# Kernel tuning notes

Measured on AMD Instinct MI355X. Metric: run time of the kernel, lower is better.

Reference implementation:

```python
import jax, jax.numpy as jnp
import numpy as np

DIM = 1536   # model dim
H = 12       # heads
HD = 128     # head dim
S = 3072     # tokens
BLK = 128    # tokens per attention block (window partition size)
NB = S // BLK  # 24 blocks
BH, BW = 6, 4  # spatial block grid (BH*BW == NB, one frame)
WIN = 6      # local window in blocks
TOPK = 128   # top-k block pairs kept per (head, frame)
EPS = 1e-5
SCALE = 1.0 / np.sqrt(HD)


def rmsnorm(x, g):
    return x * jax.lax.rsqrt(jnp.mean(x * x, axis=-1, keepdims=True) + EPS) * g


def rope(x, cos, sin):
    # x: [B,S,DIM]; cos/sin: [S,1,HD//2] -> complex rotation on (real,imag) pairs
    b, s, _ = x.shape
    x = x.reshape(b, s, H, HD // 2, 2)
    xr, xi = x[..., 0], x[..., 1]
    c, sn = cos[None], sin[None]            # [1,S,1,HD//2]
    yr = xr * c - xi * sn
    yi = xr * sn + xi * c
    return jnp.stack([yr, yi], axis=-1).reshape(b, s, H * HD)


def local_block_mask(bh, bw, win):
    # build_local_block_mask_shifted_vec_normal_slide (static, numpy)
    r, c = np.arange(bh), np.arange(bw)
    YY, XX = np.meshgrid(r, c, indexing='ij')
    ra, ca = YY.reshape(-1), XX.reshape(-1)
    hh, hw = win // 2, win // 2
    sr, sc = ra - hh, ca - hw
    er, ec = sr + win - 1, sc + win - 1
    in_r = (ra[None, :] >= sr[:, None]) & (ra[None, :] <= er[:, None])
    in_c = (ca[None, :] >= sc[:, None]) & (ca[None, :] <= ec[:, None])
    return jnp.asarray(in_r & in_c)  # [NB,NB] bool


LOCAL = local_block_mask(BH, BW, WIN)


def draft_block_mask(q, k):
    # generate_draft_block_mask: pooled-QK softmax + per-(head,frame) top-k threshold
    qw = q[0].reshape(NB, BLK, DIM).mean(axis=1)   # [NB,DIM] avgpool over window
    kw = k[0].reshape(NB, BLK, DIM).mean(axis=1)
    qh = qw.reshape(NB, H, HD).transpose(1, 0, 2)  # [H,NB,HD]
    kh = kw.reshape(NB, H, HD).transpose(1, 0, 2)
    scores = jnp.einsum('hld,hmd->hlm', qh, kh) * SCALE  # [H,NB,NB]
    rl, rn = NB // LOCAL.shape[0], NB // LOCAL.shape[1]
    lm = jnp.tile(LOCAL, (rl, rn))                       # [NB,NB]
    scores = jnp.where(lm[None], scores, -jnp.inf)
    attn = jax.nn.softmax(scores, axis=-1)               # rows include self -> finite
    it = 1  # one frame: NB == BH*BW
    flat = attn.reshape(H * it, -1)                      # [H, NB*NB]
    k_top = min(flat.shape[1] - 1, TOPK)
    thr = jax.lax.top_k(flat, k_top + 1)[0][:, -1:]      # (topk+1)-th value
    return (flat > thr).reshape(H, NB, NB)               # bool block mask


def forward(x, wq, bq, wk, bk, wv, bv, wo, bo, gq, gk, freqs_cos, freqs_sin):
    q = rope(rmsnorm(x @ wq.T + bq, gq), freqs_cos, freqs_sin)
    k = rope(rmsnorm(x @ wk.T + bk, gk), freqs_cos, freqs_sin)
    v = x @ wv.T + bv

    bm = jax.lax.stop_gradient(draft_block_mask(q, k))   # [H,NB,NB] (no-grad in torch)
    tok = jnp.repeat(jnp.repeat(bm, BLK, axis=1), BLK, axis=2)  # [H,S,S] token mask

    qh = q.reshape(1, S, H, HD).transpose(0, 2, 1, 3)
    kh = k.reshape(1, S, H, HD).transpose(0, 2, 1, 3)
    vh = v.reshape(1, S, H, HD).transpose(0, 2, 1, 3)

    s = jnp.einsum('bhsd,bhtd->bhst', qh, kh) * SCALE
    s = jnp.where(tok[None], s, -jnp.inf)
    m = jnp.max(s, axis=-1, keepdims=True)
    m = jnp.where(jnp.isfinite(m), m, 0.0)               # guard fully-masked rows
    p = jnp.exp(s - m) * tok[None].astype(s.dtype)
    den = jnp.sum(p, axis=-1, keepdims=True)
    o = jnp.einsum('bhst,bhtd->bhsd', p, vh) / jnp.where(den > 0, den, 1.0)
    o = o.transpose(0, 2, 1, 3).reshape(1, S, DIM)
    return o @ wo.T + bo


def setup_inputs() -> dict:
    key = jax.random.key(0)
    ks = jax.random.split(key, 8)
    w = lambda kk: (jax.random.normal(kk, (DIM, DIM), jnp.float32) * 0.02)
    pos = jnp.arange(S, dtype=jnp.float32)
    inv = 1.0 / (10000.0 ** (jnp.arange(HD // 2, dtype=jnp.float32) / (HD // 2)))
    ang = pos[:, None] * inv[None, :]                    # [S,HD//2]
    return {
        'x': jax.random.normal(ks[0], (1, S, DIM), jnp.float32),
        'wq': w(ks[1]), 'bq': jnp.zeros((DIM,), jnp.float32),
        'wk': w(ks[2]), 'bk': jnp.zeros((DIM,), jnp.float32),
        'wv': w(ks[3]), 'bv': jnp.zeros((DIM,), jnp.float32),
        'wo': w(ks[4]), 'bo': jnp.zeros((DIM,), jnp.float32),
        'gq': jnp.ones((DIM,), jnp.float32),
        'gk': jnp.ones((DIM,), jnp.float32),
        'freqs_cos': jnp.cos(ang)[:, None, :],
        'freqs_sin': jnp.sin(ang)[:, None, :],
    }


def reference(x, wq, bq, wk, bk, wv, bv, wo, bo, gq, gk, freqs_cos, freqs_sin):
    return forward(x, wq, bq, wk, bk, wv, bv, wo, bo, gq, gk, freqs_cos, freqs_sin)
```

## Files before the change

### kernel.cpp

```cpp
#include <hip/hip_runtime.h>
#include <hip/hip_bf16.h>
#include <math.h>

#define SEQ 3072
#define DIM 1536
#define NH 12
#define HD 128
#define NB 24
#define BLKT 128
#define NBSQ 576
#define TOPK_N 128
#define EPSV 1e-5f
#define SCALEV 0.08838834764831845f

typedef __attribute__((ext_vector_type(8))) short short8;
typedef __attribute__((ext_vector_type(4))) short short4v;
typedef __attribute__((ext_vector_type(4))) float f32x4;

typedef __attribute__((address_space(1))) void* gas1_t;
typedef __attribute__((address_space(3))) void* las3_t;

__device__ __forceinline__ float b2f(short u) {
  return __uint_as_float(((unsigned int)(unsigned short)u) << 16);
}
__device__ __forceinline__ short f2b(float x) {
  __hip_bfloat16 h = __float2bfloat16(x);
  return *reinterpret_cast<short*>(&h);
}
__device__ __forceinline__ float ldin(const void* p, size_t i, int f32) {
  return f32 ? ((const float*)p)[i] : b2f(((const short*)p)[i]);
}
__device__ __forceinline__ void gload_lds16(const void* g, void* l) {
  __builtin_amdgcn_global_load_lds((gas1_t)g, (las3_t)l, 16, 0, 0);
}

__global__ __launch_bounds__(256)
void dtype_probe(const void* __restrict__ w, int* __restrict__ flag) {
  __shared__ int cnt;
  if (threadIdx.x == 0) cnt = 0;
  __syncthreads();
  const short* p = (const short*)w;
  int local = 0;
  for (int i = threadIdx.x; i < 4096; i += 256) {
    float v = b2f(p[i]);
    if (!(fabsf(v) <= 1e3f)) local++;
  }
  atomicAdd(&cnt, local);
  __syncthreads();
  if (threadIdx.x == 0) { flag[0] = (cnt > 16) ? 1 : 0; flag[1] = 0; }
}

__device__ __forceinline__ short8 ldchunk(const void* __restrict__ p, size_t idx, int f32) {
  if (f32) {
    const float* q = (const float*)p + idx;
    f32x4 a = *(const f32x4*)q;
    f32x4 b = *(const f32x4*)(q + 4);
    short8 r;
    r[0] = f2b(a[0]); r[1] = f2b(a[1]); r[2] = f2b(a[2]); r[3] = f2b(a[3]);
    r[4] = f2b(b[0]); r[5] = f2b(b[1]); r[6] = f2b(b[2]); r[7] = f2b(b[3]);
    return r;
  }
  return *(const short8*)((const short*)p + idx);
}

__global__ __launch_bounds__(256)
void cvt_bf16(const void* __restrict__ in, short* __restrict__ out, int n8,
              const int* __restrict__ f) {
  int i = blockIdx.x * 256 + threadIdx.x;
  if (i >= n8) return;
  *(short8*)(out + (size_t)i * 8) = ldchunk(in, (size_t)i * 8, *f);
}

#define BK 64

__global__ __launch_bounds__(256)
void gemm128(const short* __restrict__ A,
             const void* __restrict__ W0, const void* __restrict__ W1, const void* __restrict__ W2,
             const void* __restrict__ b0, const void* __restrict__ b1, const void* __restrict__ b2,
             void* __restrict__ C0, void* __restrict__ C1, void* __restrict__ C2,
             int useWB, const int* __restrict__ wfp, const int* __restrict__ ofp) {
  const int fW = *wfp, fO = *ofp;
  __shared__ __attribute__((aligned(16))) short As[128 * BK];
  __shared__ __attribute__((aligned(16))) short Bs[128 * BK];
  const int tid = threadIdx.x;
  const int w = tid >> 6, lane = tid & 63;
  const int lo = lane & 15, hi = lane >> 4;
  const int wr = w >> 1, wc = w & 1;
  const int bx = blockIdx.x;
  const int wsel = bx / 12;
  const int col0 = (bx - wsel * 12) * 128;
  const int row0 = blockIdx.y * 128;
  const void* W = (wsel == 0) ? W0 : ((wsel == 1) ? W1 : W2);
  const void* bb = (wsel == 0) ? b0 : ((wsel == 1) ? b1 : b2);
  void* C = (wsel == 0) ? C0 : ((wsel == 1) ? C1 : C2);

  const f32x4 zero = {0.f, 0.f, 0.f, 0.f};
  f32x4 acc[4][4];
#pragma unroll
  for (int i = 0; i < 4; i++)
#pragma unroll
    for (int j = 0; j < 4; j++) acc[i][j] = zero;

  for (int k0 = 0; k0 < DIM; k0 += BK) {
#pragma unroll
    for (int i = 0; i < 4; i++) {
      int id = i * 256 + tid;
      int r = id >> 3, c = id & 7;
      gload_lds16(A + (size_t)(row0 + r) * DIM + k0 + (c ^ (r & 7)) * 8, &As[id * 8]);
    }
    if (useWB) {
#pragma unroll
      for (int i = 0; i < 4; i++) {
        int id = i * 256 + tid;
        int r = id >> 3, c = id & 7;
        gload_lds16((const short*)W + (size_t)(col0 + r) * DIM + k0 + (c ^ (r & 7)) * 8,
                    &Bs[id * 8]);
      }
    } else {
#pragma unroll
      for (int i = 0; i < 4; i++) {
        int id = i * 256 + tid;
        int r = id >> 3, c = id & 7;
        short8 v = ldchunk(W, (size_t)(col0 + r) * DIM + k0 + c * 8, fW);
        *(short8*)&Bs[r * BK + 8 * (c ^ (r & 7))] = v;
      }
    }
    __syncthreads();
#pragma unroll
    for (int kk = 0; kk < 2; kk++) {
      short8 av[4], bv[4];
#pragma unroll
      for (int mi = 0; mi < 4; mi++) {
        int r = wr * 64 + mi * 16 + lo;
        av[mi] = *(const short8*)&As[r * BK + 8 * ((kk * 4 + hi) ^ (r & 7))];
      }
#pragma unroll
      for (int ni = 0; ni < 4; ni++) {
        int r = wc * 64 + ni * 16 + lo;
        bv[ni] = *(const short8*)&Bs[r * BK + 8 * ((kk * 4 + hi) ^ (r & 7))];
      }
#pragma unroll
      for (int mi = 0; mi < 4; mi++)
#pragma unroll
        for (int ni = 0; ni < 4; ni++)
          acc[mi][ni] = __builtin_amdgcn_mfma_f32_16x16x32_bf16(av[mi], bv[ni], acc[mi][ni], 0, 0, 0);
    }
    __syncthreads();
  }

#pragma unroll
  for (int ni = 0; ni < 4; ni++) {
    int col = col0 + wc * 64 + ni * 16 + lo;
    float bias = ldin(bb, col, fW);
#pragma unroll
    for (int mi = 0; mi < 4; mi++) {
      int rowb = row0 + wr * 64 + mi * 16 + hi * 4;
#pragma unroll
      for (int g = 0; g < 4; g++) {
        float v = acc[mi][ni][g] + bias;
        size_t oi = (size_t)(rowb + g) * DIM + col;
        if (fO) ((float*)C)[oi] = v;
        else    ((short*)C)[oi] = f2b(v);
      }
    }
  }
}

__global__ __launch_bounds__(256)
void rmsnorm_rope_kernel(short* __restrict__ x, const void* __restrict__ g,
                         const void* __restrict__ cs, const void* __restrict__ sn,
                         const int* __restrict__ f) {
  const int fI = *f;
  const int s = blockIdx.x, tid = threadIdx.x;
  short* row = x + (size_t)s * DIM;
  short8 rv = {};
  float ss = 0.f;
  if (tid < 192) {
    rv = *(const short8*)(row + tid * 8);
#pragma unroll
    for (int j = 0; j < 8; j++) { float v = b2f(rv[j]); ss += v * v; }
  }
#pragma unroll
  for (int m = 32; m; m >>= 1) ss += __shfl_xor(ss, m, 64);
  __shared__ float wsum[4];
  if ((tid & 63) == 0) wsum[tid >> 6] = ss;
  __syncthreads();
  float rn = rsqrtf((wsum[0] + wsum[1] + wsum[2] + wsum[3]) * (1.0f / DIM) + EPSV);
  if (tid >= 192) return;
  short8 out;
#pragma unroll
  for (int j = 0; j < 4; j++) {
    int p = tid * 4 + j, pi = p & 63;
    float c  = ldin(cs, (size_t)s * 64 + pi, fI);
    float si = ldin(sn, (size_t)s * 64 + pi, fI);
    float xr = b2f(rv[2 * j])     * rn * ldin(g, tid * 8 + 2 * j, fI);
    float xi = b2f(rv[2 * j + 1]) * rn * ldin(g, tid * 8 + 2 * j + 1, fI);
    out[2 * j]     = f2b(xr * c - xi * si);
    out[2 * j + 1] = f2b(xr * si + xi * c);
  }
  *(short8*)(row + tid * 8) = out;
}

__global__ __launch_bounds__(256)
void pool_kernel(const short* __restrict__ x, float* __restrict__ out) {
  const int nb = blockIdx.x;
  const int d = blockIdx.y * 256 + threadIdx.x;
  float s = 0.f;
  for (int t = 0; t < BLKT; t++) s += b2f(x[(size_t)(nb * BLKT + t) * DIM + d]);
  out[nb * DIM + d] = s * (1.0f / BLKT);
}

__global__ __launch_bounds__(256)
void draft_mask_kernel(const float* __restrict__ qw, const float* __restrict__ kw,
                       int* __restrict__ bm) {
  const int h = blockIdx.x, tid = threadIdx.x;
  __shared__ float qh[NB][HD];
  __shared__ float kh[NB][HD];
  __shared__ float attn[NBSQ];
  __shared__ int cw[4];

  for (int idx = tid; idx < NB * HD; idx += 256) {
    int l = idx >> 7, d = idx & 127;
    qh[l][d] = qw[l * DIM + h * HD + d];
    kh[l][d] = kw[l * DIM + h * HD + d];
  }
  __syncthreads();

  for (int idx = tid; idx < NBSQ; idx += 256) {
    int l = idx / NB, m = idx % NB;
    int rl = l >> 2, cl = l & 3, rm = m >> 2, cm = m & 3;
    bool loc = (rm >= rl - 3) && (rm <= rl + 2) && (cm >= cl - 3) && (cm <= cl + 2);
    float sc;
    if (loc) {
      sc = 0.f;
      for (int d = 0; d < HD; d++) sc += qh[l][d] * kh[m][d];
      sc *= SCALEV;
    } else {
      sc = -INFINITY;
    }
    attn[idx] = sc;
  }
  __syncthreads();

  if (tid < NB) {
    float mx = -INFINITY;
    for (int m = 0; m < NB; m++) mx = fmaxf(mx, attn[tid * NB + m]);
    float sm = 0.f;
    for (int m = 0; m < NB; m++) {
      float p = expf(attn[tid * NB + m] - mx);
      attn[tid * NB + m] = p;
      sm += p;
    }
    float inv = 1.0f / sm;
    for (int m = 0; m < NB; m++) attn[tid * NB + m] *= inv;
  }
  __syncthreads();

  unsigned int blo = 0u, bhi = 0x3F800000u;
  while (blo < bhi) {
    unsigned int mid = (blo + bhi) >> 1;
    float t = __uint_as_float(mid);
    int c = 0;
    for (int idx = tid; idx < NBSQ; idx += 256) c += (attn[idx] > t) ? 1 : 0;
#pragma unroll
    for (int m = 1; m < 64; m <<= 1) c += __shfl_xor(c, m, 64);
    if ((tid & 63) == 0) cw[tid >> 6] = c;
    __syncthreads();
    int tot = cw[0] + cw[1] + cw[2] + cw[3];
    if (tot <= TOPK_N) bhi = mid; else blo = mid + 1;
    __syncthreads();
  }
  float thr = __uint_as_float(blo);

  for (int idx = tid; idx < NBSQ; idx += 256)
    bm[h * NBSQ + idx] = (attn[idx] > thr) ? 1 : 0;
}

__global__ __launch_bounds__(256)
void transpose_kernel(const short* __restrict__ v, short* __restrict__ vt) {
  __shared__ short tile[64][68];
  const int s0 = blockIdx.x * 64, c0 = blockIdx.y * 64;
  const int tid = threadIdx.x;
#pragma unroll
  for (int i = 0; i < 4; i++) {
    int id = i * 256 + tid;
    int r = id >> 4, cq = (id & 15) * 4;
    *(short4v*)&tile[r][cq] = *(const short4v*)(v + (size_t)(s0 + r) * DIM + c0 + cq);
  }
  __syncthreads();
#pragma unroll
  for (int i = 0; i < 4; i++) {
    int id = i * 256 + tid;
    int d = id >> 4, sq = (id & 15) * 4;
    short4v val;
#pragma unroll
    for (int jj = 0; jj < 4; jj++) val[jj] = tile[sq + jj][d];
    *(short4v*)(vt + (size_t)(c0 + d) * SEQ + s0 + sq) = val;
  }
}

__global__ __launch_bounds__(512)
void attn_mfma(const short* __restrict__ q, const short* __restrict__ k,
               const short* __restrict__ vt, const int* __restrict__ bm,
               short* __restrict__ o, int* __restrict__ ctr) {
  const int xcd = blockIdx.x & 7;
  const int tid = threadIdx.x;
  const int w = tid >> 6;
  const int lane = tid & 63;
  const int lo = lane & 15, hi = lane >> 4;

  __shared__ __attribute__((aligned(16))) short Ks[128 * 128];
  __shared__ __attribute__((aligned(16))) short Vs[128 * 128];
  __shared__ __attribute__((aligned(16))) short Ps[8][16 * 128];
  __shared__ int tsh;

  const f32x4 zero = {0.f, 0.f, 0.f, 0.f};
  const int sr = tid >> 4, sc = tid & 15;

  for (;;) {
    if (tid == 0) tsh = atomicAdd(&ctr[xcd * 8], 1);
    __syncthreads();
    const int slot = tsh;
    if (slot >= 36) break;
    const int task = xcd * 36 + slot;
    const int h = task / NB;
    const int qb = task - h * NB;

    const int* bmrow = bm + h * NBSQ + qb * NB;
    const short* kh = k + h * HD;
    const short* vth = vt + (size_t)h * HD * SEQ;

    const int qt = qb * 8 + w;
    const int qrow = qt * 16 + lo;
    short8 qa[4];
#pragma unroll
    for (int kk = 0; kk < 4; kk++)
      qa[kk] = *(const short8*)(q + (size_t)qrow * DIM + h * HD + kk * 32 + hi * 8);

    f32x4 oacc[8];
#pragma unroll
    for (int i = 0; i < 8; i++) oacc[i] = zero;
    float m_i[4] = {-INFINITY, -INFINITY, -INFINITY, -INFINITY};
    float l_i[4] = {0.f, 0.f, 0.f, 0.f};

    short8 kreg[4], vreg[4];
    int jc = 0;
    while (jc < NB && !bmrow[jc]) jc++;
    if (jc < NB) {
      const int t0 = jc * BLKT;
#pragma unroll
      for (int i = 0; i < 4; i++) {
        int r = i * 32 + sr;
        kreg[i] = *(const short8*)(kh + (size_t)(t0 + r) * DIM + sc * 8);
        vreg[i] = *(const short8*)(vth + (size_t)r * SEQ + t0 + sc * 8);
      }
    }

    while (jc < NB) {
#pragma unroll
      for (int i = 0; i < 4; i++) {
        int r = i * 32 + sr;
        *(short8*)&Ks[r * 128 + 8 * (sc ^ (r & 7))] = kreg[i];
        *(short8*)&Vs[r * 128 + 8 * (sc ^ (r & 7))] = vreg[i];
      }
      __syncthreads();

      int jn = jc + 1;
      while (jn < NB && !bmrow[jn]) jn++;
      if (jn < NB) {
        const int t0 = jn * BLKT;
#pragma unroll
        for (int i = 0; i < 4; i++) {
          int r = i * 32 + sr;
          kreg[i] = *(const short8*)(kh + (size_t)(t0 + r) * DIM + sc * 8);
          vreg[i] = *(const short8*)(vth + (size_t)r * SEQ + t0 + sc * 8);
        }
      }

      f32x4 S[8];
#pragma unroll
      for (int tt = 0; tt < 8; tt++) {
        f32x4 s = zero;
#pragma unroll
        for (int kk = 0; kk < 4; kk++) {
          int rt = tt * 16 + lo;
          short8 kb = *(const short8*)&Ks[rt * 128 + 8 * ((kk * 4 + hi) ^ (rt & 7))];
          s = __builtin_amdgcn_mfma_f32_16x16x32_bf16(qa[kk], kb, s, 0, 0, 0);
        }
        S[tt] = s;
      }

      float alpha[4];
#pragma unroll
      for (int g = 0; g < 4; g++) {
        float mx = S[0][g];
#pragma unroll
        for (int tt = 1; tt < 8; tt++) mx = fmaxf(mx, S[tt][g]);
#pragma unroll
        for (int msk = 1; msk < 16; msk <<= 1) mx = fmaxf(mx, __shfl_xor(mx, msk, 16));
        mx *= SCALEV;
        float mn = fmaxf(m_i[g], mx);
        alpha[g] = __expf(m_i[g] - mn);
        float ps = 0.f;
        int r = hi * 4 + g;
#pragma unroll
        for (int tt = 0; tt < 8; tt++) {
          float p = __expf(S[tt][g] * SCALEV - mn);
          ps += p;
          int t = tt * 16 + lo;
          Ps[w][r * 128 + 8 * ((t >> 3) ^ (r & 7)) + (t & 7)] = f2b(p);
        }
#pragma unroll
        for (int msk = 1; msk < 16; msk <<= 1) ps += __shfl_xor(ps, msk, 16);
        l_i[g] = l_i[g] * alpha[g] + ps;
        m_i[g] = mn;
      }
#pragma unroll
      for (int dt = 0; dt < 8; dt++) {
        f32x4 t = oacc[dt];
        t[0] *= alpha[0]; t[1] *= alpha[1]; t[2] *= alpha[2]; t[3] *= alpha[3];
        oacc[dt] = t;
      }

#pragma unroll
      for (int kk = 0; kk < 4; kk++) {
        int ch = kk * 4 + hi;
        short8 pa = *(const short8*)&Ps[w][lo * 128 + 8 * (ch ^ (lo & 7))];
#pragma unroll
        for (int dt = 0; dt < 8; dt++) {
          int rd = dt * 16 + lo;
          short8 vb = *(const short8*)&Vs[rd * 128 + 8 * (ch ^ (rd & 7))];
          oacc[dt] = __builtin_amdgcn_mfma_f32_16x16x32_bf16(pa, vb, oacc[dt], 0, 0, 0);
        }
      }
      __syncthreads();
      jc = jn;
    }

    float inv[4];
#pragma unroll
    for (int g = 0; g < 4; g++) inv[g] = (l_i[g] > 0.f) ? 1.f / l_i[g] : 0.f;
#pragma unroll
    for (int dt = 0; dt < 8; dt++)
#pragma unroll
      for (int g = 0; g < 4; g++)
        o[(size_t)(qt * 16 + hi * 4 + g) * DIM + h * HD + dt * 16 + lo] =
            f2b(oacc[dt][g] * inv[g]);
    __syncthreads();
  }
}

extern "C" void kernel_launch(void* const* d_in, const int* in_sizes, int n_in,
                              void* d_out, int out_size, void* d_ws, size_t ws_size,
                              hipStream_t stream) {
  char* wsb = (char*)d_ws;
  int*   flag = (int*)(wsb + 0);
  int*   ctr  = (int*)(wsb + 64);
  float* qw   = (float*)(wsb + 512);
  float* kw   = (float*)(wsb + 512 + 147456);
  int*   bm   = (int*)(wsb + 512 + 294912);
  const size_t base = 323072;
  short* q16 = (short*)(wsb + base);
  short* k16 = q16 + (size_t)SEQ * DIM;
  short* v16 = k16 + (size_t)SEQ * DIM;
  short* xb  = v16 + (size_t)SEQ * DIM;
  short* vt  = xb;
  short* o16 = v16;

  const int bigws = (ws_size >= (size_t)56 * 1024 * 1024) ? 1 : 0;
  short* wqb = xb + (size_t)SEQ * DIM;
  short* wkb = wqb + (size_t)DIM * DIM;
  short* wvb = wkb + (size_t)DIM * DIM;
  short* wob = wqb;

  dtype_probe<<<1, 256, 0, stream>>>(d_in[1], flag);
  hipMemsetAsync(ctr, 0, 256, stream);

  const int n8x = SEQ * DIM / 8;
  const int n8w = DIM * DIM / 8;
  cvt_bf16<<<n8x / 256, 256, 0, stream>>>(d_in[0], xb, n8x, flag);
  if (bigws) {
    cvt_bf16<<<n8w / 256, 256, 0, stream>>>(d_in[1], wqb, n8w, flag);
    cvt_bf16<<<n8w / 256, 256, 0, stream>>>(d_in[3], wkb, n8w, flag);
    cvt_bf16<<<n8w / 256, 256, 0, stream>>>(d_in[5], wvb, n8w, flag);
  }

  gemm128<<<dim3(36, SEQ / 128), 256, 0, stream>>>(
      xb,
      bigws ? (const void*)wqb : d_in[1],
      bigws ? (const void*)wkb : d_in[3],
      bigws ? (const void*)wvb : d_in[5],
      d_in[2], d_in[4], d_in[6],
      q16, k16, v16,
      bigws, flag, flag + 1);

  rmsnorm_rope_kernel<<<SEQ, 256, 0, stream>>>(q16, d_in[9],  d_in[11], d_in[12], flag);
  rmsnorm_rope_kernel<<<SEQ, 256, 0, stream>>>(k16, d_in[10], d_in[11], d_in[12], flag);

  pool_kernel<<<dim3(NB, DIM / 256), 256, 0, stream>>>(q16, qw);
  pool_kernel<<<dim3(NB, DIM / 256), 256, 0, stream>>>(k16, kw);

  draft_mask_kernel<<<NH, 256, 0, stream>>>(qw, kw, bm);

  transpose_kernel<<<dim3(SEQ / 64, DIM / 64), 256, 0, stream>>>(v16, vt);
  if (bigws) cvt_bf16<<<n8w / 256, 256, 0, stream>>>(d_in[7], wob, n8w, flag);

  attn_mfma<<<256, 512, 0, stream>>>(q16, k16, vt, bm, o16, ctr);

  gemm128<<<dim3(12, SEQ / 128), 256, 0, stream>>>(
      o16,
      bigws ? (const void*)wob : d_in[7], bigws ? (const void*)wob : d_in[7],
      bigws ? (const void*)wob : d_in[7],
      d_in[8], d_in[8], d_in[8],
      d_out, d_out, d_out,
      bigws, flag, flag);
}
```

Before: 374.4 us.

## Split attention tasks into half-blocks and schedule longest-first per XCD

```diff
diff --git a/kernel.cpp b/kernel.cpp
--- a/kernel.cpp
+++ b/kernel.cpp
@@ -212,7 +212,7 @@
 
 __global__ __launch_bounds__(256)
 void draft_mask_kernel(const float* __restrict__ qw, const float* __restrict__ kw,
-                       int* __restrict__ bm) {
+                       int* __restrict__ bm, int* __restrict__ cost) {
   const int h = blockIdx.x, tid = threadIdx.x;
   __shared__ float qh[NB][HD];
   __shared__ float kh[NB][HD];
@@ -274,6 +274,29 @@
 
   for (int idx = tid; idx < NBSQ; idx += 256)
     bm[h * NBSQ + idx] = (attn[idx] > thr) ? 1 : 0;
+
+  if (tid < NB) {
+    int cnt = 0;
+    for (int m = 0; m < NB; m++) cnt += (attn[tid * NB + m] > thr) ? 1 : 0;
+    cost[h * NB + tid] = cnt;
+  }
+}
+
+__global__ __launch_bounds__(256)
+void order_tasks(const int* __restrict__ cost, int* __restrict__ taskmap) {
+  int t = blockIdx.x * 256 + threadIdx.x;
+  if (t >= 576) return;
+  int xcd = t / 72, base = xcd * 72;
+  int h = t / 48, rem = t - h * 48, l = rem >> 1;
+  int c = cost[h * NB + l];
+  int rank = 0;
+  for (int j = 0; j < 72; j++) {
+    int tj = base + j;
+    int hj = tj / 48, remj = tj - hj * 48, lj = remj >> 1;
+    int cj = cost[hj * NB + lj];
+    if (cj > c || (cj == c && tj < t)) rank++;
+  }
+  taskmap[base + rank] = t;
 }
 
 __global__ __launch_bounds__(256)
@@ -299,10 +322,11 @@
   }
 }
 
-__global__ __launch_bounds__(512)
+__global__ __launch_bounds__(256)
 void attn_mfma(const short* __restrict__ q, const short* __restrict__ k,
                const short* __restrict__ vt, const int* __restrict__ bm,
-               short* __restrict__ o, int* __restrict__ ctr) {
+               short* __restrict__ o, int* __restrict__ ctr,
+               const int* __restrict__ taskmap) {
   const int xcd = blockIdx.x & 7;
   const int tid = threadIdx.x;
   const int w = tid >> 6;
@@ -311,7 +335,7 @@
 
   __shared__ __attribute__((aligned(16))) short Ks[128 * 128];
   __shared__ __attribute__((aligned(16))) short Vs[128 * 128];
-  __shared__ __attribute__((aligned(16))) short Ps[8][16 * 128];
+  __shared__ __attribute__((aligned(16))) short Ps[4][16 * 128];
   __shared__ int tsh;
 
   const f32x4 zero = {0.f, 0.f, 0.f, 0.f};
@@ -321,16 +345,17 @@
     if (tid == 0) tsh = atomicAdd(&ctr[xcd * 8], 1);
     __syncthreads();
     const int slot = tsh;
-    if (slot >= 36) break;
-    const int task = xcd * 36 + slot;
-    const int h = task / NB;
-    const int qb = task - h * NB;
-
-    const int* bmrow = bm + h * NBSQ + qb * NB;
+    if (slot >= 72) break;
+    const int t = taskmap[xcd * 72 + slot];
+    const int h = t / 48;
+    const int rem = t - h * 48;
+    const int l = rem >> 1, half = rem & 1;
+
+    const int* bmrow = bm + h * NBSQ + l * NB;
     const short* kh = k + h * HD;
     const short* vth = vt + (size_t)h * HD * SEQ;
 
-    const int qt = qb * 8 + w;
+    const int qt = l * 8 + half * 4 + w;
     const int qrow = qt * 16 + lo;
     short8 qa[4];
 #pragma unroll
@@ -343,14 +368,14 @@
     float m_i[4] = {-INFINITY, -INFINITY, -INFINITY, -INFINITY};
     float l_i[4] = {0.f, 0.f, 0.f, 0.f};
 
-    short8 kreg[4], vreg[4];
+    short8 kreg[8], vreg[8];
     int jc = 0;
     while (jc < NB && !bmrow[jc]) jc++;
     if (jc < NB) {
       const int t0 = jc * BLKT;
 #pragma unroll
-      for (int i = 0; i < 4; i++) {
-        int r = i * 32 + sr;
+      for (int i = 0; i < 8; i++) {
+        int r = i * 16 + sr;
         kreg[i] = *(const short8*)(kh + (size_t)(t0 + r) * DIM + sc * 8);
         vreg[i] = *(const short8*)(vth + (size_t)r * SEQ + t0 + sc * 8);
       }
@@ -358,8 +383,8 @@
 
     while (jc < NB) {
 #pragma unroll
-      for (int i = 0; i < 4; i++) {
-        int r = i * 32 + sr;
+      for (int i = 0; i < 8; i++) {
+        int r = i * 16 + sr;
         *(short8*)&Ks[r * 128 + 8 * (sc ^ (r & 7))] = kreg[i];
         *(short8*)&Vs[r * 128 + 8 * (sc ^ (r & 7))] = vreg[i];
       }
@@ -370,8 +395,8 @@
       if (jn < NB) {
         const int t0 = jn * BLKT;
 #pragma unroll
-        for (int i = 0; i < 4; i++) {
-          int r = i * 32 + sr;
+        for (int i = 0; i < 8; i++) {
+          int r = i * 16 + sr;
           kreg[i] = *(const short8*)(kh + (size_t)(t0 + r) * DIM + sc * 8);
           vreg[i] = *(const short8*)(vth + (size_t)r * SEQ + t0 + sc * 8);
         }
@@ -407,8 +432,8 @@
         for (int tt = 0; tt < 8; tt++) {
           float p = __expf(S[tt][g] * SCALEV - mn);
           ps += p;
-          int t = tt * 16 + lo;
-          Ps[w][r * 128 + 8 * ((t >> 3) ^ (r & 7)) + (t & 7)] = f2b(p);
+          int t2 = tt * 16 + lo;
+          Ps[w][r * 128 + 8 * ((t2 >> 3) ^ (r & 7)) + (t2 & 7)] = f2b(p);
         }
 #pragma unroll
         for (int msk = 1; msk < 16; msk <<= 1) ps += __shfl_xor(ps, msk, 16);
@@ -417,9 +442,9 @@
       }
 #pragma unroll
       for (int dt = 0; dt < 8; dt++) {
-        f32x4 t = oacc[dt];
-        t[0] *= alpha[0]; t[1] *= alpha[1]; t[2] *= alpha[2]; t[3] *= alpha[3];
-        oacc[dt] = t;
+        f32x4 tv = oacc[dt];
+        tv[0] *= alpha[0]; tv[1] *= alpha[1]; tv[2] *= alpha[2]; tv[3] *= alpha[3];
+        oacc[dt] = tv;
       }
 
 #pragma unroll
@@ -456,10 +481,12 @@
   char* wsb = (char*)d_ws;
   int*   flag = (int*)(wsb + 0);
   int*   ctr  = (int*)(wsb + 64);
-  float* qw   = (float*)(wsb + 512);
-  float* kw   = (float*)(wsb + 512 + 147456);
-  int*   bm   = (int*)(wsb + 512 + 294912);
-  const size_t base = 323072;
+  int*   cost = (int*)(wsb + 384);
+  int*   tmap = (int*)(wsb + 1536);
+  float* qw   = (float*)(wsb + 4096);
+  float* kw   = (float*)(wsb + 4096 + 147456);
+  int*   bm   = (int*)(wsb + 4096 + 294912);
+  const size_t base = 327680;
   short* q16 = (short*)(wsb + base);
   short* k16 = q16 + (size_t)SEQ * DIM;
   short* v16 = k16 + (size_t)SEQ * DIM;
@@ -500,12 +527,13 @@
   pool_kernel<<<dim3(NB, DIM / 256), 256, 0, stream>>>(q16, qw);
   pool_kernel<<<dim3(NB, DIM / 256), 256, 0, stream>>>(k16, kw);
 
-  draft_mask_kernel<<<NH, 256, 0, stream>>>(qw, kw, bm);
+  draft_mask_kernel<<<NH, 256, 0, stream>>>(qw, kw, bm, cost);
+  order_tasks<<<3, 256, 0, stream>>>(cost, tmap);
 
   transpose_kernel<<<dim3(SEQ / 64, DIM / 64), 256, 0, stream>>>(v16, vt);
   if (bigws) cvt_bf16<<<n8w / 256, 256, 0, stream>>>(d_in[7], wob, n8w, flag);
 
-  attn_mfma<<<256, 512, 0, stream>>>(q16, k16, vt, bm, o16, ctr);
+  attn_mfma<<<512, 256, 0, stream>>>(q16, k16, vt, bm, o16, ctr, tmap);
 
   gemm128<<<dim3(12, SEQ / 128), 256, 0, stream>>>(
       o16,
```

After: 376.1 us. About the same (+0.4%).
